# Kernel tuning notes

Measured on AMD Instinct MI355X. Metric: run time of the kernel, lower is better.

The kernel has to match this reference:

```python
import jax, jax.numpy as jnp
import numpy as np

NFEAT, NHID = 128, 128

def setup_inputs() -> dict:
    key = jax.random.key(0)
    k1, k2, k3, k4 = jax.random.split(key, 4)
    x = jax.random.normal(k1, (32, 1024, NFEAT), dtype=jnp.float32)
    adj = jax.random.uniform(k2, (32, 1024, 1024), dtype=jnp.float32)
    # GraphConvolution parameters (Kipf init ~ uniform, scale irrelevant for correctness)
    bound = 1.0 / np.sqrt(NHID)
    W = jax.random.uniform(k3, (NFEAT, NHID), dtype=jnp.float32, minval=-bound, maxval=bound)
    b = jax.random.uniform(k4, (NHID,), dtype=jnp.float32, minval=-bound, maxval=bound)
    return {"x": x, "adj": adj, "W": W, "b": b}

def reference(x, adj, W, b):
    # Batched equivalent of the per-sample python loop:
    # out[i] = relu(adj[i] @ (x[i] @ W) + b); dropout is identity in eval mode.
    support = jnp.einsum('bnf,fh->bnh', x, W)          # [B, N, nhid]
    out = jnp.einsum('bnm,bmh->bnh', adj, support) + b  # [B, N, nhid]
    return jax.nn.relu(out)
```

## Files before the change

kernel.cpp:

```cpp
#include <hip/hip_runtime.h>
#include <hip/hip_bf16.h>
#include <stdint.h>


typedef short bf16x8 __attribute__((ext_vector_type(8)));
typedef float f32x4 __attribute__((ext_vector_type(4)));
typedef unsigned short u16x4 __attribute__((ext_vector_type(4)));

__device__ __forceinline__ unsigned short f2bf(float f) {
    uint32_t u = __builtin_bit_cast(uint32_t, f);
    u += 0x7FFFu + ((u >> 16) & 1u);
    return (unsigned short)(u >> 16);
}

__device__ __forceinline__ bf16x8 cvt8(f32x4 v0, f32x4 v1) {
    union { __hip_bfloat162 h[4]; bf16x8 v; } u;
    u.h[0] = __float22bfloat162_rn(make_float2(v0.x, v0.y));
    u.h[1] = __float22bfloat162_rn(make_float2(v0.z, v0.w));
    u.h[2] = __float22bfloat162_rn(make_float2(v1.x, v1.y));
    u.h[3] = __float22bfloat162_rn(make_float2(v1.z, v1.w));
    return u.v;
}

#define K1S 136
__global__ __launch_bounds__(256) void k1_support(const float* __restrict__ x,
                                                  const float* __restrict__ W,
                                                  unsigned short* __restrict__ ST) {
    __shared__ __align__(16) unsigned short xt[64 * K1S];
    __shared__ __align__(16) unsigned short wt[128 * K1S];
    int t = threadIdx.x;
    int node_base = blockIdx.x * 64;

    const f32x4* xg = (const f32x4*)(x + (size_t)node_base * 128);
#pragma unroll
    for (int i = 0; i < 8; ++i) {
        int f4 = i * 256 + t;
        int row = f4 >> 5, c4 = f4 & 31;
        f32x4 v = xg[f4];
        u16x4 p;
        p.x = f2bf(v.x); p.y = f2bf(v.y); p.z = f2bf(v.z); p.w = f2bf(v.w);
        *(u16x4*)&xt[row * K1S + c4 * 4] = p;
    }
#pragma unroll
    for (int i = 0; i < 16; ++i) {
        int c = i * 256 + t;
        int f = c >> 5, h4 = c & 31;
        f32x4 v = *(const f32x4*)(W + f * 128 + h4 * 4);
        wt[(h4 * 4 + 0) * K1S + f] = f2bf(v.x);
        wt[(h4 * 4 + 1) * K1S + f] = f2bf(v.y);
        wt[(h4 * 4 + 2) * K1S + f] = f2bf(v.z);
        wt[(h4 * 4 + 3) * K1S + f] = f2bf(v.w);
    }
    __syncthreads();

    int wv = t >> 6, lane = t & 63, l16 = lane & 15, quad = lane >> 4;
    int wave_h = (wv & 1) * 64, wave_m = (wv >> 1) * 32;

    f32x4 acc[4][2];
#pragma unroll
    for (int ht = 0; ht < 4; ++ht)
#pragma unroll
        for (int mt = 0; mt < 2; ++mt) acc[ht][mt] = 0.f;

#pragma unroll
    for (int s = 0; s < 4; ++s) {
        int ko = s * 32 + quad * 8;
        bf16x8 a[4], bb[2];
#pragma unroll
        for (int ht = 0; ht < 4; ++ht)
            a[ht] = *(const bf16x8*)&wt[(wave_h + ht * 16 + l16) * K1S + ko];
#pragma unroll
        for (int mt = 0; mt < 2; ++mt)
            bb[mt] = *(const bf16x8*)&xt[(wave_m + mt * 16 + l16) * K1S + ko];
#pragma unroll
        for (int ht = 0; ht < 4; ++ht)
#pragma unroll
            for (int mt = 0; mt < 2; ++mt)
                acc[ht][mt] = __builtin_amdgcn_mfma_f32_16x16x32_bf16(
                    a[ht], bb[mt], acc[ht][mt], 0, 0, 0);
    }

    int batch = blockIdx.x >> 4;
    int m_in_b = (blockIdx.x & 15) * 64;
#pragma unroll
    for (int ht = 0; ht < 4; ++ht)
#pragma unroll
        for (int mt = 0; mt < 2; ++mt) {
            int mcol = wave_m + mt * 16 + l16;
#pragma unroll
            for (int r = 0; r < 4; ++r) {
                int h = wave_h + ht * 16 + quad * 4 + r;
                ST[(((size_t)batch * 128 + h) << 10) + m_in_b + mcol] =
                    f2bf(acc[ht][mt][r]);
            }
        }
}

__global__ __launch_bounds__(256) void k2_gcn(const float* __restrict__ adj,
                                              const unsigned short* __restrict__ ST,
                                              const float* __restrict__ bias,
                                              float* __restrict__ out) {
    const int t = threadIdx.x;
    const int wv = t >> 6, l = t & 63, l16 = l & 15, quad = l >> 4;
    const int batch = blockIdx.x >> 4;
    const int mbase = (blockIdx.x & 15) * 64;
    const int wave_m = (wv & 1) * 32, wave_n = (wv >> 1) * 64;

    const float* pA[2];
    const unsigned short* pB[4];
#pragma unroll
    for (int i = 0; i < 2; ++i)
        pA[i] = adj + ((size_t)(batch * 1024 + mbase + wave_m + i * 16 + l16) * 1024
                       + quad * 8);
#pragma unroll
    for (int j = 0; j < 4; ++j)
        pB[j] = ST + ((size_t)(batch * 128 + wave_n + j * 16 + l16) * 1024
                      + quad * 8);

    float bv[4];
#pragma unroll
    for (int j = 0; j < 4; ++j) bv[j] = bias[wave_n + j * 16 + l16];

    f32x4 acc[2][4];
#pragma unroll
    for (int i = 0; i < 2; ++i)
#pragma unroll
        for (int j = 0; j < 4; ++j) acc[i][j] = 0.f;

#pragma unroll 4
    for (int kc = 0; kc < 32; ++kc) {
        bf16x8 a[2], bb[4];
#pragma unroll
        for (int i = 0; i < 2; ++i) {
            f32x4 v0 = *(const f32x4*)(pA[i] + kc * 32);
            f32x4 v1 = *(const f32x4*)(pA[i] + kc * 32 + 4);
            a[i] = cvt8(v0, v1);
        }
#pragma unroll
        for (int j = 0; j < 4; ++j)
            bb[j] = *(const bf16x8*)(pB[j] + kc * 32);
#pragma unroll
        for (int i = 0; i < 2; ++i)
#pragma unroll
            for (int j = 0; j < 4; ++j)
                acc[i][j] = __builtin_amdgcn_mfma_f32_16x16x32_bf16(
                    a[i], bb[j], acc[i][j], 0, 0, 0);
    }

    float* outb = out + ((size_t)batch * 1024 + mbase) * 128;
#pragma unroll
    for (int i = 0; i < 2; ++i)
#pragma unroll
        for (int j = 0; j < 4; ++j) {
            int n = wave_n + j * 16 + l16;
#pragma unroll
            for (int r = 0; r < 4; ++r) {
                int m = wave_m + i * 16 + quad * 4 + r;
                float v = acc[i][j][r] + bv[j];
                outb[(size_t)m * 128 + n] = fmaxf(v, 0.f);
            }
        }
}

extern "C" void kernel_launch(void* const* d_in, const int* in_sizes, int n_in,
                              void* d_out, int out_size, void* d_ws, size_t ws_size,
                              hipStream_t stream) {
    const float* x = (const float*)d_in[0];
    const float* adj = (const float*)d_in[1];
    const float* W = (const float*)d_in[2];
    const float* b = (const float*)d_in[3];
    float* out = (float*)d_out;

    unsigned short* ST = (unsigned short*)d_ws;

    k1_support<<<512, 256, 0, stream>>>(x, W, ST);
    k2_gcn<<<512, 256, 0, stream>>>(adj, ST, b, out);
}
```

Measured before the change: 253.3 us.

## Stage adj rows into swizzled LDS as bf16 with coalesced loads in GCN kernel

The aggregation kernel now loads each block's 32 full adj rows with coalesced float4 reads, converts them to bf16, and stores them in a 64KB XOR-swizzled shared tile before running the MFMA loop. Previously each lane read 32-byte strided chunks across rows directly from global memory. Block tile shrinks to 32 rows and the grid doubles, which reduces per-wave work and doubles reads of the support matrix. The large LDS footprint limits occupancy, and there is no overlap between the load phase and compute.

```diff
diff --git a/kernel.cpp b/kernel.cpp
--- a/kernel.cpp
+++ b/kernel.cpp
@@ -11,15 +11,6 @@
     uint32_t u = __builtin_bit_cast(uint32_t, f);
     u += 0x7FFFu + ((u >> 16) & 1u);
     return (unsigned short)(u >> 16);
-}
-
-__device__ __forceinline__ bf16x8 cvt8(f32x4 v0, f32x4 v1) {
-    union { __hip_bfloat162 h[4]; bf16x8 v; } u;
-    u.h[0] = __float22bfloat162_rn(make_float2(v0.x, v0.y));
-    u.h[1] = __float22bfloat162_rn(make_float2(v0.z, v0.w));
-    u.h[2] = __float22bfloat162_rn(make_float2(v1.x, v1.y));
-    u.h[3] = __float22bfloat162_rn(make_float2(v1.z, v1.w));
-    return u.v;
 }
 
 #define K1S 136
@@ -100,66 +91,67 @@
                                               const unsigned short* __restrict__ ST,
                                               const float* __restrict__ bias,
                                               float* __restrict__ out) {
+    __shared__ __align__(16) unsigned short As[32 * 1024];
     const int t = threadIdx.x;
     const int wv = t >> 6, l = t & 63, l16 = l & 15, quad = l >> 4;
-    const int batch = blockIdx.x >> 4;
-    const int mbase = (blockIdx.x & 15) * 64;
-    const int wave_m = (wv & 1) * 32, wave_n = (wv >> 1) * 64;
+    const int batch = blockIdx.x >> 5;
+    const int mbase = (blockIdx.x & 31) * 32;
 
-    const float* pA[2];
+    const float* adjb = adj + ((size_t)batch * 1024 + mbase) * 1024;
+
+    {
+        const int c = t >> 1, half = (t & 1) * 4;
+#pragma unroll 8
+        for (int i = 0; i < 32; ++i) {
+            f32x4 v = *(const f32x4*)(adjb + (size_t)i * 1024 + t * 4);
+            u16x4 p;
+            p.x = f2bf(v.x); p.y = f2bf(v.y); p.z = f2bf(v.z); p.w = f2bf(v.w);
+            *(u16x4*)&As[i * 1024 + ((c ^ (i & 7)) << 3) + half] = p;
+        }
+    }
+    __syncthreads();
+
+    const int wave_m = (wv & 1) * 16, wave_n = (wv >> 1) * 64;
     const unsigned short* pB[4];
 #pragma unroll
-    for (int i = 0; i < 2; ++i)
-        pA[i] = adj + ((size_t)(batch * 1024 + mbase + wave_m + i * 16 + l16) * 1024
-                       + quad * 8);
-#pragma unroll
     for (int j = 0; j < 4; ++j)
-        pB[j] = ST + ((size_t)(batch * 128 + wave_n + j * 16 + l16) * 1024
-                      + quad * 8);
+        pB[j] = ST + ((size_t)(batch * 128 + wave_n + j * 16 + l16)) * 1024 + quad * 8;
 
     float bv[4];
 #pragma unroll
     for (int j = 0; j < 4; ++j) bv[j] = bias[wave_n + j * 16 + l16];
 
-    f32x4 acc[2][4];
+    f32x4 acc[4];
 #pragma unroll
-    for (int i = 0; i < 2; ++i)
-#pragma unroll
-        for (int j = 0; j < 4; ++j) acc[i][j] = 0.f;
+    for (int j = 0; j < 4; ++j) acc[j] = 0.f;
 
-#pragma unroll 4
+    const int ar = wave_m + l16;
+    const unsigned short* arow = &As[ar * 1024];
+    const int akey = ar & 7;
+
+#pragma unroll 8
     for (int kc = 0; kc < 32; ++kc) {
-        bf16x8 a[2], bb[4];
-#pragma unroll
-        for (int i = 0; i < 2; ++i) {
-            f32x4 v0 = *(const f32x4*)(pA[i] + kc * 32);
-            f32x4 v1 = *(const f32x4*)(pA[i] + kc * 32 + 4);
-            a[i] = cvt8(v0, v1);
-        }
+        bf16x8 a = *(const bf16x8*)&arow[(((kc * 4 + quad) ^ akey) << 3)];
+        bf16x8 bb[4];
 #pragma unroll
         for (int j = 0; j < 4; ++j)
             bb[j] = *(const bf16x8*)(pB[j] + kc * 32);
 #pragma unroll
-        for (int i = 0; i < 2; ++i)
-#pragma unroll
-            for (int j = 0; j < 4; ++j)
-                acc[i][j] = __builtin_amdgcn_mfma_f32_16x16x32_bf16(
-                    a[i], bb[j], acc[i][j], 0, 0, 0);
+        for (int j = 0; j < 4; ++j)
+            acc[j] = __builtin_amdgcn_mfma_f32_16x16x32_bf16(a, bb[j], acc[j], 0, 0, 0);
     }
 
     float* outb = out + ((size_t)batch * 1024 + mbase) * 128;
 #pragma unroll
-    for (int i = 0; i < 2; ++i)
+    for (int j = 0; j < 4; ++j) {
+        int n = wave_n + j * 16 + l16;
 #pragma unroll
-        for (int j = 0; j < 4; ++j) {
-            int n = wave_n + j * 16 + l16;
-#pragma unroll
-            for (int r = 0; r < 4; ++r) {
-                int m = wave_m + i * 16 + quad * 4 + r;
-                float v = acc[i][j][r] + bv[j];
-                outb[(size_t)m * 128 + n] = fmaxf(v, 0.f);
-            }
+        for (int r = 0; r < 4; ++r) {
+            int m = wave_m + quad * 4 + r;
+            float v = acc[j][r] + bv[j];
+            outb[(size_t)m * 128 + n] = fmaxf(v, 0.f);
         }
+    }
 }
 
 extern "C" void kernel_launch(void* const* d_in, const int* in_sizes, int n_in,
@@ -174,5 +166,5 @@
     unsigned short* ST = (unsigned short*)d_ws;
 
     k1_support<<<512, 256, 0, stream>>>(x, W, ST);
-    k2_gcn<<<512, 256, 0, stream>>>(adj, ST, b, out);
+    k2_gcn<<<1024, 256, 0, stream>>>(adj, ST, b, out);
 }
```

Measured after the change: 270.8 us. +6.9%, slower.
